# Optimization experiments

Measured on AMD Instinct MI355X. Metric: run time of the kernel, lower is better.

## Reference

```python
import jax, jax.numpy as jnp
import numpy as np

C, T, H, W, K = 12, 10, 4, 7, 3  # hardcoded in the original forward
PAD = 1
EPS = 1e-5


def setup_inputs() -> dict:
    key = jax.random.key(0)
    ks = jax.random.split(key, 14)
    nt = 32768
    x = jax.random.normal(ks[0], (nt, C, T, H * W), jnp.float32)
    # G: Linear(T -> 2T) -> BN1d(2T) -> ReLU -> Linear(2T -> K) -> Softmax
    w_g1 = jax.random.normal(ks[1], (2 * T, T), jnp.float32) * 0.3
    g1_gamma = 1.0 + 0.1 * jax.random.normal(ks[2], (2 * T,), jnp.float32)
    g1_beta = 0.1 * jax.random.normal(ks[3], (2 * T,), jnp.float32)
    g1_mean = 0.1 * jax.random.normal(ks[4], (2 * T,), jnp.float32)
    g1_var = jax.random.uniform(ks[5], (2 * T,), jnp.float32, 0.5, 1.5)
    w_g2 = jax.random.normal(ks[6], (K, 2 * T), jnp.float32) * 0.3
    # L: Conv1d(C -> C//4, K) -> BN1d(C//4) -> ReLU -> Conv1d(C//4 -> C, 1) -> Sigmoid
    w_l1 = jax.random.normal(ks[7], (C // 4, C, K), jnp.float32) * 0.3
    l1_gamma = 1.0 + 0.1 * jax.random.normal(ks[8], (C // 4,), jnp.float32)
    l1_beta = 0.1 * jax.random.normal(ks[9], (C // 4,), jnp.float32)
    l1_mean = 0.1 * jax.random.normal(ks[10], (C // 4,), jnp.float32)
    l1_var = jax.random.uniform(ks[11], (C // 4,), jnp.float32, 0.5, 1.5)
    w_l2 = jax.random.normal(ks[12], (C, C // 4, 1), jnp.float32) * 0.3
    return dict(x=x, w_g1=w_g1, g1_gamma=g1_gamma, g1_beta=g1_beta,
                g1_mean=g1_mean, g1_var=g1_var, w_g2=w_g2, w_l1=w_l1,
                l1_gamma=l1_gamma, l1_beta=l1_beta, l1_mean=l1_mean,
                l1_var=l1_var, w_l2=w_l2)


def reference(x, w_g1, g1_gamma, g1_beta, g1_mean, g1_var, w_g2,
              w_l1, l1_gamma, l1_beta, l1_mean, l1_var, w_l2):
    n = x.shape[0]
    new_x = x.reshape(n, C, T, H, W)
    # adaptive_avg_pool2d((1,1)) == mean over spatial dims -> [n, C, T]
    pooled = new_x.mean(axis=(3, 4))
    # --- G branch: per-(sample,channel) temporal kernel, [n, C, K] ---
    rows = pooled.reshape(n * C, T)
    z = rows @ w_g1.T
    z = (z - g1_mean) * jax.lax.rsqrt(g1_var + EPS) * g1_gamma + g1_beta
    z = jax.nn.relu(z)
    kern = jax.nn.softmax(z @ w_g2.T, axis=-1).reshape(n, C, K)
    # --- L branch: local channel-temporal gating, [n, C, T] ---
    a = jax.lax.conv_general_dilated(pooled, w_l1, (1,), [(K // 2, K // 2)],
                                     dimension_numbers=('NCH', 'OIH', 'NCH'))
    a = (a - l1_mean[None, :, None]) * jax.lax.rsqrt(l1_var + EPS)[None, :, None] \
        * l1_gamma[None, :, None] + l1_beta[None, :, None]
    a = jax.nn.relu(a)
    a = jax.lax.conv_general_dilated(a, w_l2, (1,), [(0, 0)],
                                     dimension_numbers=('NCH', 'OIH', 'NCH'))
    act = jax.nn.sigmoid(a)  # [n, C, T]
    # --- modulate and apply per-(sample,channel) depthwise temporal conv ---
    xm = new_x * act[:, :, :, None, None]  # [n, C, T, H, W]
    xp = jnp.pad(xm, ((0, 0), (0, 0), (PAD, PAD), (0, 0), (0, 0)))
    out = kern[:, :, 0, None, None, None] * xp[:, :, 0:T]
    for j in range(1, K):  # K=3, tiny structural loop
        out = out + kern[:, :, j, None, None, None] * xp[:, :, j:j + T]
    # permute [n,c,t,h,w] -> [n,t,c,h,w] and flatten time into batch
    out = jnp.transpose(out, (0, 2, 1, 3, 4)).reshape(n * T, C, H, W)
    return out
```

## Files before the change

kernel.cpp:

```cpp
#include <hip/hip_runtime.h>


#define CC 12
#define TT 10
#define SAMPLE 3360
#define SAMPLE4 840
#define EPSF 1e-5f

typedef float f4 __attribute__((ext_vector_type(4)));

__global__ __launch_bounds__(256) void tam_kernel(
    const float* __restrict__ x,
    const float* __restrict__ w_g1,
    const float* __restrict__ g1_gamma, const float* __restrict__ g1_beta,
    const float* __restrict__ g1_mean,  const float* __restrict__ g1_var,
    const float* __restrict__ w_g2,
    const float* __restrict__ w_l1,
    const float* __restrict__ l1_gamma, const float* __restrict__ l1_beta,
    const float* __restrict__ l1_mean,  const float* __restrict__ l1_var,
    const float* __restrict__ w_l2,
    float* __restrict__ out)
{
    __shared__ f4    sx4[SAMPLE4];
    __shared__ float spool[120];
    __shared__ float sz[240];
    __shared__ float sa1[30];
    __shared__ float skern[36];
    __shared__ float sact[120];
    __shared__ float wg1s[200], wg2s[60], wl1s[108], wl2s[36];
    __shared__ float gs[20], gb[20], lsc[3], lbi[3];

    const int n   = blockIdx.x;
    const int tid = threadIdx.x;

    const f4* xg = reinterpret_cast<const f4*>(x + (size_t)n * SAMPLE);
    for (int v = tid; v < SAMPLE4; v += 256) sx4[v] = xg[v];
    for (int i = tid; i < 200; i += 256) wg1s[i] = w_g1[i];
    if (tid < 60)  wg2s[tid] = w_g2[tid];
    if (tid < 108) wl1s[tid] = w_l1[tid];
    if (tid < 36)  wl2s[tid] = w_l2[tid];
    if (tid < 20) {
        const float s = rsqrtf(g1_var[tid] + EPSF) * g1_gamma[tid];
        gs[tid] = s; gb[tid] = g1_beta[tid] - g1_mean[tid] * s;
    } else if (tid < 23) {
        const int m = tid - 20;
        const float s = rsqrtf(l1_var[m] + EPSF) * l1_gamma[m];
        lsc[m] = s; lbi[m] = l1_beta[m] - l1_mean[m] * s;
    }
    __syncthreads();

    if (tid < 120) {
        const f4* rp = sx4 + tid * 7;
        f4 a = rp[0];
        #pragma unroll
        for (int i = 1; i < 7; ++i) a += rp[i];
        spool[tid] = (a.x + a.y + a.z + a.w) * (1.0f / 28.0f);
    }
    __syncthreads();

    for (int task = tid; task < 270; task += 256) {
        if (task < 240) {
            const int c = task / 20, j = task % 20;
            float s = 0.f;
            #pragma unroll
            for (int t = 0; t < TT; ++t)
                s += spool[c * TT + t] * wg1s[j * TT + t];
            sz[task] = fmaxf(gs[j] * s + gb[j], 0.f);
        } else {
            const int e = task - 240;
            const int m = e / TT, t = e % TT;
            float s = 0.f;
            #pragma unroll
            for (int c = 0; c < CC; ++c) {
                #pragma unroll
                for (int k = 0; k < 3; ++k) {
                    const int t2 = t + k - 1;
                    if (t2 >= 0 && t2 < TT)
                        s += spool[c * TT + t2] * wl1s[(m * CC + c) * 3 + k];
                }
            }
            sa1[e] = fmaxf(lsc[m] * s + lbi[m], 0.f);
        }
    }
    __syncthreads();

    if (tid < CC) {
        const int c = tid;
        float sc0 = 0.f, sc1 = 0.f, sc2 = 0.f;
        #pragma unroll
        for (int j = 0; j < 20; ++j) {
            const float zj = sz[c * 20 + j];
            sc0 += zj * wg2s[j];
            sc1 += zj * wg2s[20 + j];
            sc2 += zj * wg2s[40 + j];
        }
        const float mx = fmaxf(sc0, fmaxf(sc1, sc2));
        const float e0 = __expf(sc0 - mx), e1 = __expf(sc1 - mx), e2 = __expf(sc2 - mx);
        const float ri = 1.0f / (e0 + e1 + e2);
        skern[c]      = e0 * ri;
        skern[12 + c] = e1 * ri;
        skern[24 + c] = e2 * ri;
    }
    if (tid >= 64 && tid < 64 + 120) {
        const int idx = tid - 64;
        const int c = idx / TT, t = idx % TT;
        float s = 0.f;
        #pragma unroll
        for (int m = 0; m < 3; ++m) s += sa1[m * TT + t] * wl2s[c * 3 + m];
        sact[idx] = 1.0f / (1.0f + __expf(-s));
    }
    __syncthreads();

    f4* og = reinterpret_cast<f4*>(out + (size_t)n * SAMPLE);
    for (int v = tid; v < SAMPLE4; v += 256) {
        const int t   = v / 84;
        const int rem = v % 84;
        const int c   = rem / 7;
        const int s4  = rem % 7;
        const int base = c * 70 + s4;
        const float k0 = skern[c];
        const float k1 = skern[12 + c];
        const float k2 = skern[24 + c];
        f4 acc = (k1 * sact[c * TT + t]) * sx4[base + t * 7];
        if (t > 0)
            acc += (k0 * sact[c * TT + t - 1]) * sx4[base + (t - 1) * 7];
        if (t < TT - 1)
            acc += (k2 * sact[c * TT + t + 1]) * sx4[base + (t + 1) * 7];
        __builtin_nontemporal_store(acc, og + v);
    }
}

extern "C" void kernel_launch(void* const* d_in, const int* in_sizes, int n_in,
                              void* d_out, int out_size, void* d_ws, size_t ws_size,
                              hipStream_t stream) {
    (void)n_in; (void)out_size; (void)d_ws; (void)ws_size;
    const float* x        = (const float*)d_in[0];
    const float* w_g1     = (const float*)d_in[1];
    const float* g1_gamma = (const float*)d_in[2];
    const float* g1_beta  = (const float*)d_in[3];
    const float* g1_mean  = (const float*)d_in[4];
    const float* g1_var   = (const float*)d_in[5];
    const float* w_g2     = (const float*)d_in[6];
    const float* w_l1     = (const float*)d_in[7];
    const float* l1_gamma = (const float*)d_in[8];
    const float* l1_beta  = (const float*)d_in[9];
    const float* l1_mean  = (const float*)d_in[10];
    const float* l1_var   = (const float*)d_in[11];
    const float* w_l2     = (const float*)d_in[12];
    float* out = (float*)d_out;

    const int n_total = in_sizes[0] / SAMPLE;
    tam_kernel<<<n_total, 256, 0, stream>>>(
        x, w_g1, g1_gamma, g1_beta, g1_mean, g1_var, w_g2,
        w_l1, l1_gamma, l1_beta, l1_mean, l1_var, w_l2, out);
}
```

Before: 206.9 us.

## Compute gating redundantly per wavefront to replace block barriers with wave syncs

Each of the four wavefronts now computes the pooled means, G/L branch MLPs, softmax kernel and sigmoid gate itself in a private scratch area. This replaces three block-wide __syncthreads with wave-local LDS waits, keeping one block barrier after the tile load. The x tile is loaded into registers first and then stored to LDS with a padded per-channel row stride, which reduces bank conflicts during pooling. The cost is four times the small gating arithmetic and extra LDS scratch per block, which may lower occupancy.

Result: slower. 280.6 us (+35.6%).

```diff
diff --git a/kernel.cpp b/kernel.cpp
--- a/kernel.cpp
+++ b/kernel.cpp
@@ -5,9 +5,17 @@
 #define TT 10
 #define SAMPLE 3360
 #define SAMPLE4 840
+#define CROW 71
 #define EPSF 1e-5f
 
 typedef float f4 __attribute__((ext_vector_type(4)));
+
+#define FENCE() __builtin_amdgcn_sched_barrier(0)
+#define WSYNC() do { asm volatile("s_waitcnt lgkmcnt(0)" ::: "memory"); FENCE(); } while (0)
+#define BLOCK_SYNC() do { asm volatile("s_waitcnt lgkmcnt(0)" ::: "memory"); \
+    FENCE(); __builtin_amdgcn_s_barrier(); FENCE(); } while (0)
+
+#define SCR 426
 
 __global__ __launch_bounds__(256) void tam_kernel(
     const float* __restrict__ x,
@@ -21,20 +29,24 @@
     const float* __restrict__ w_l2,
     float* __restrict__ out)
 {
-    __shared__ f4    sx4[SAMPLE4];
-    __shared__ float spool[120];
-    __shared__ float sz[240];
-    __shared__ float sa1[30];
-    __shared__ float skern[36];
-    __shared__ float sact[120];
+    __shared__ f4    sx4[CC * CROW];
     __shared__ float wg1s[200], wg2s[60], wl1s[108], wl2s[36];
     __shared__ float gs[20], gb[20], lsc[3], lbi[3];
+    __shared__ float wscr[4][SCR];
 
-    const int n   = blockIdx.x;
-    const int tid = threadIdx.x;
+    const int n    = blockIdx.x;
+    const int tid  = threadIdx.x;
+    const int wid  = tid >> 6;
+    const int lane = tid & 63;
+    float* p = wscr[wid];
 
     const f4* xg = reinterpret_cast<const f4*>(x + (size_t)n * SAMPLE);
-    for (int v = tid; v < SAMPLE4; v += 256) sx4[v] = xg[v];
+    f4 r[4];
+    #pragma unroll
+    for (int k = 0; k < 4; ++k) {
+        const int v = tid + k * 256;
+        if (v < SAMPLE4) r[k] = xg[v];
+    }
     for (int i = tid; i < 200; i += 256) wg1s[i] = w_g1[i];
     if (tid < 60)  wg2s[tid] = w_g2[tid];
     if (tid < 108) wl1s[tid] = w_l1[tid];
@@ -47,26 +59,41 @@
         const float s = rsqrtf(l1_var[m] + EPSF) * l1_gamma[m];
         lsc[m] = s; lbi[m] = l1_beta[m] - l1_mean[m] * s;
     }
-    __syncthreads();
+    #pragma unroll
+    for (int k = 0; k < 4; ++k) {
+        const int v = tid + k * 256;
+        if (v < SAMPLE4) {
+            const int c = v / 70, rm = v % 70;
+            sx4[c * CROW + rm] = r[k];
+        }
+    }
+    BLOCK_SYNC();
 
-    if (tid < 120) {
-        const f4* rp = sx4 + tid * 7;
-        f4 a = rp[0];
-        #pragma unroll
-        for (int i = 1; i < 7; ++i) a += rp[i];
-        spool[tid] = (a.x + a.y + a.z + a.w) * (1.0f / 28.0f);
+    #pragma unroll
+    for (int q = 0; q < 2; ++q) {
+        const int row = lane + q * 64;
+        if (row < 120) {
+            const int c = row / 10, t = row % 10;
+            const f4* rp = sx4 + c * CROW + t * 7;
+            f4 a = rp[0];
+            #pragma unroll
+            for (int i = 1; i < 7; ++i) a += rp[i];
+            p[row] = (a.x + a.y + a.z + a.w) * (1.0f / 28.0f);
+        }
     }
-    __syncthreads();
+    WSYNC();
 
-    for (int task = tid; task < 270; task += 256) {
+    #pragma unroll
+    for (int q = 0; q < 5; ++q) {
+        const int task = lane + q * 64;
         if (task < 240) {
             const int c = task / 20, j = task % 20;
             float s = 0.f;
             #pragma unroll
             for (int t = 0; t < TT; ++t)
-                s += spool[c * TT + t] * wg1s[j * TT + t];
-            sz[task] = fmaxf(gs[j] * s + gb[j], 0.f);
-        } else {
+                s += p[c * TT + t] * wg1s[j * TT + t];
+            p[120 + task] = fmaxf(gs[j] * s + gb[j], 0.f);
+        } else if (task < 270) {
             const int e = task - 240;
             const int m = e / TT, t = e % TT;
             float s = 0.f;
@@ -76,57 +103,64 @@
                 for (int k = 0; k < 3; ++k) {
                     const int t2 = t + k - 1;
                     if (t2 >= 0 && t2 < TT)
-                        s += spool[c * TT + t2] * wl1s[(m * CC + c) * 3 + k];
+                        s += p[c * TT + t2] * wl1s[(m * CC + c) * 3 + k];
                 }
             }
-            sa1[e] = fmaxf(lsc[m] * s + lbi[m], 0.f);
+            p[360 + e] = fmaxf(lsc[m] * s + lbi[m], 0.f);
         }
     }
-    __syncthreads();
+    WSYNC();
 
-    if (tid < CC) {
-        const int c = tid;
-        float sc0 = 0.f, sc1 = 0.f, sc2 = 0.f;
-        #pragma unroll
-        for (int j = 0; j < 20; ++j) {
-            const float zj = sz[c * 20 + j];
-            sc0 += zj * wg2s[j];
-            sc1 += zj * wg2s[20 + j];
-            sc2 += zj * wg2s[40 + j];
+    #pragma unroll
+    for (int q = 0; q < 3; ++q) {
+        const int task = lane + q * 64;
+        if (task < CC) {
+            const int c = task;
+            float sc0 = 0.f, sc1 = 0.f, sc2 = 0.f;
+            #pragma unroll
+            for (int j = 0; j < 20; ++j) {
+                const float zj = p[120 + c * 20 + j];
+                sc0 += zj * wg2s[j];
+                sc1 += zj * wg2s[20 + j];
+                sc2 += zj * wg2s[40 + j];
+            }
+            const float mx = fmaxf(sc0, fmaxf(sc1, sc2));
+            const float e0 = __expf(sc0 - mx), e1 = __expf(sc1 - mx), e2 = __expf(sc2 - mx);
+            const float ri = 1.0f / (e0 + e1 + e2);
+            p[390 + c]      = e0 * ri;
+            p[402 + c]      = e1 * ri;
+            p[414 + c]      = e2 * ri;
+        } else if (task < 12 + 120) {
+            const int e = task - 12;
+            const int c = e / TT, t = e % TT;
+            float s = 0.f;
+            #pragma unroll
+            for (int m = 0; m < 3; ++m) s += p[360 + m * TT + t] * wl2s[c * 3 + m];
+            p[e] = 1.0f / (1.0f + __expf(-s));
         }
-        const float mx = fmaxf(sc0, fmaxf(sc1, sc2));
-        const float e0 = __expf(sc0 - mx), e1 = __expf(sc1 - mx), e2 = __expf(sc2 - mx);
-        const float ri = 1.0f / (e0 + e1 + e2);
-        skern[c]      = e0 * ri;
-        skern[12 + c] = e1 * ri;
-        skern[24 + c] = e2 * ri;
     }
-    if (tid >= 64 && tid < 64 + 120) {
-        const int idx = tid - 64;
-        const int c = idx / TT, t = idx % TT;
-        float s = 0.f;
-        #pragma unroll
-        for (int m = 0; m < 3; ++m) s += sa1[m * TT + t] * wl2s[c * 3 + m];
-        sact[idx] = 1.0f / (1.0f + __expf(-s));
-    }
-    __syncthreads();
+    WSYNC();
 
     f4* og = reinterpret_cast<f4*>(out + (size_t)n * SAMPLE);
-    for (int v = tid; v < SAMPLE4; v += 256) {
-        const int t   = v / 84;
-        const int rem = v % 84;
-        const int c   = rem / 7;
-        const int s4  = rem % 7;
-        const int base = c * 70 + s4;
-        const float k0 = skern[c];
-        const float k1 = skern[12 + c];
-        const float k2 = skern[24 + c];
-        f4 acc = (k1 * sact[c * TT + t]) * sx4[base + t * 7];
-        if (t > 0)
-            acc += (k0 * sact[c * TT + t - 1]) * sx4[base + (t - 1) * 7];
-        if (t < TT - 1)
-            acc += (k2 * sact[c * TT + t + 1]) * sx4[base + (t + 1) * 7];
-        __builtin_nontemporal_store(acc, og + v);
+    #pragma unroll
+    for (int k = 0; k < 4; ++k) {
+        const int v = tid + k * 256;
+        if (v < SAMPLE4) {
+            const int t   = v / 84;
+            const int rem = v % 84;
+            const int c   = rem / 7;
+            const int s4  = rem % 7;
+            const int base = c * CROW + s4;
+            const float k0 = p[390 + c];
+            const float k1 = p[402 + c];
+            const float k2 = p[414 + c];
+            f4 acc = (k1 * p[c * TT + t]) * sx4[base + t * 7];
+            if (t > 0)
+                acc += (k0 * p[c * TT + t - 1]) * sx4[base + (t - 1) * 7];
+            if (t < TT - 1)
+                acc += (k2 * p[c * TT + t + 1]) * sx4[base + (t + 1) * 7];
+            __builtin_nontemporal_store(acc, og + v);
+        }
     }
 }
 
```
